# Kernel tuning notes

Measured on AMD Instinct MI355X. Metric: run time of the kernel, lower is better.

The kernel has to match this reference:

```python
import jax, jax.numpy as jnp
import numpy as np

IN_FEATURES = 4096
OUT_FEATURES = 2048
N_GROUPS = 16  # group size = IN_FEATURES // N_GROUPS = 256


def setup_inputs() -> dict:
    key = jax.random.key(0)
    k1, k2, k3, k4 = jax.random.split(key, 4)
    x = jax.random.normal(k1, (8, 64, IN_FEATURES), dtype=jnp.float32)
    # uint8 quantized weights, stored [out, in] as in the torch module
    qweight = jax.random.randint(k2, (OUT_FEATURES, IN_FEATURES), 0, 256).astype(jnp.uint8)
    # per-(out-channel, group) dequant scale and offset; scale ~ (max-min)/255 of rand weights
    qrange = jax.random.uniform(k3, (OUT_FEATURES, N_GROUPS), dtype=jnp.float32) * (2.0 / 255.0)
    qmin = -jax.random.uniform(k4, (OUT_FEATURES, N_GROUPS), dtype=jnp.float32)
    return {"x": x, "qweight": qweight, "qrange": qrange, "qmin": qmin}


def reference(x, qweight, qrange, qmin):
    # out[b,s,o] = sum_i x[b,s,i] * (q[o,i]*qrange[o,g(i)] + qmin[o,g(i)])
    B, S, IN = x.shape
    OUT, G = qrange.shape
    gs = IN // G
    xg = x.reshape(B, S, G, gs)                     # [B,S,G,gs]
    qg = qweight.reshape(OUT, G, gs).astype(x.dtype)  # [O,G,gs]
    # fused per-group dequant matmul: scale folded into the contraction
    out = jnp.einsum('bsgi,ogi,og->bso', xg, qg, qrange)
    # offset term: qmin[o,g] * sum_i_in_group x[b,s,i]
    out = out + jnp.einsum('bsg,og->bso', xg.sum(axis=-1), qmin)
    return out
```

## Files before the change

### kernel.cpp

```cpp
#include <hip/hip_runtime.h>
#include <hip/hip_bf16.h>


#define M_T 512
#define N_T 2048
#define K_T 4096
#define NGRP 16
#define BM 128
#define BN 128
#define BK 64
#define OUT_ELEMS (M_T * N_T)
#define W_ELEMS (N_T * K_T)
#define X_ELEMS (M_T * K_T)

typedef __attribute__((ext_vector_type(8))) short mfrag_t;
typedef __attribute__((ext_vector_type(8))) unsigned short u16x8;
typedef __attribute__((ext_vector_type(4))) float f32x4;

__device__ __forceinline__ unsigned short f2bf(float f) {
  union { __hip_bfloat16 h; unsigned short u; } c;
  c.h = __float2bfloat16(f);
  return c.u;
}

__global__ __launch_bounds__(256) void pack_kernel(
    const float* __restrict__ x, const int* __restrict__ qw,
    const float* __restrict__ qrange, const float* __restrict__ qmin,
    unsigned short* __restrict__ wsW, unsigned short* __restrict__ wsX) {
  const int bid = blockIdx.x;
  const int tid = threadIdx.x;
  if (bid < (W_ELEMS / 8) / 256) {
    const int gidx = bid * 256 + tid;
    const int o = gidx >> 9;
    const int k8 = gidx & 511;
    const int g = k8 >> 5;
    const float sc = qrange[o * NGRP + g];
    const float mn = qmin[o * NGRP + g];
    const int4* q = (const int4*)(qw + ((size_t)o << 12) + (k8 << 3));
    const int4 q0 = q[0], q1 = q[1];
    u16x8 p;
    p[0] = f2bf((float)q0.x * sc + mn); p[1] = f2bf((float)q0.y * sc + mn);
    p[2] = f2bf((float)q0.z * sc + mn); p[3] = f2bf((float)q0.w * sc + mn);
    p[4] = f2bf((float)q1.x * sc + mn); p[5] = f2bf((float)q1.y * sc + mn);
    p[6] = f2bf((float)q1.z * sc + mn); p[7] = f2bf((float)q1.w * sc + mn);
    *(u16x8*)(wsW + ((size_t)gidx << 3)) = p;
  } else {
    const int gidx = (bid - (W_ELEMS / 8) / 256) * 256 + tid;
    const float4* a = (const float4*)(x + ((size_t)gidx << 3));
    const float4 a0 = a[0], a1 = a[1];
    u16x8 p;
    p[0] = f2bf(a0.x); p[1] = f2bf(a0.y); p[2] = f2bf(a0.z); p[3] = f2bf(a0.w);
    p[4] = f2bf(a1.x); p[5] = f2bf(a1.y); p[6] = f2bf(a1.z); p[7] = f2bf(a1.w);
    *(u16x8*)(wsX + ((size_t)gidx << 3)) = p;
  }
}

template <int KSPLIT, bool XCDSWZ>
__global__ __launch_bounds__(512, 4) void dq_gemm_kernel(
    const unsigned short* __restrict__ wsX, const unsigned short* __restrict__ wsW,
    float* __restrict__ dst) {
  constexpr int KC = K_T / KSPLIT;
  constexpr int NTC = KC / BK;

  __shared__ __align__(16) unsigned short As[BM * BK];
  __shared__ __align__(16) unsigned short Bs[BN * BK];

  const int tid = threadIdx.x;
  int xt, yt, kc;
  if (XCDSWZ) {
    const int b = blockIdx.x;
    kc = b & 7;
    const int slot = b >> 3;
    xt = slot & 15;
    yt = slot >> 4;
  } else {
    const int b = blockIdx.x;
    xt = b & 15;
    yt = (b >> 4) & 3;
    kc = b >> 6;
  }
  const int n0 = xt * BN;
  const int m0 = yt * BM;
  const int kbase = kc * KC;

  const int lane = tid & 63;
  const int wv = tid >> 6;
  const int wm = (wv >> 2) * 64;
  const int wn = (wv & 3) * 32;
  const int lr = lane & 15;
  const int lq = lane >> 4;
  const int rxl = lr & 7;

  const int swzcol = (((lane & 7) ^ (lane >> 3)) << 3);
  const int r0 = wv * 16 + (lane >> 3);
  const int r1 = r0 + 8;
  const unsigned short* gA0 = wsX + (size_t)(m0 + r0) * K_T + kbase + swzcol;
  const unsigned short* gA1 = wsX + (size_t)(m0 + r1) * K_T + kbase + swzcol;
  const unsigned short* gB0 = wsW + (size_t)(n0 + r0) * K_T + kbase + swzcol;
  const unsigned short* gB1 = wsW + (size_t)(n0 + r1) * K_T + kbase + swzcol;
  unsigned short* lA0 = &As[wv * 1024];
  unsigned short* lA1 = &As[wv * 1024 + 512];
  unsigned short* lB0 = &Bs[wv * 1024];
  unsigned short* lB1 = &Bs[wv * 1024 + 512];

#define STAGE(T)                                                              \
  do {                                                                        \
    const size_t o_ = (size_t)(T) * BK;                                       \
    __builtin_amdgcn_global_load_lds(                                         \
        (const __attribute__((address_space(1))) void*)(gA0 + o_),            \
        (__attribute__((address_space(3))) void*)lA0, 16, 0, 0);              \
    __builtin_amdgcn_global_load_lds(                                         \
        (const __attribute__((address_space(1))) void*)(gA1 + o_),            \
        (__attribute__((address_space(3))) void*)lA1, 16, 0, 0);              \
    __builtin_amdgcn_global_load_lds(                                         \
        (const __attribute__((address_space(1))) void*)(gB0 + o_),            \
        (__attribute__((address_space(3))) void*)lB0, 16, 0, 0);              \
    __builtin_amdgcn_global_load_lds(                                         \
        (const __attribute__((address_space(1))) void*)(gB1 + o_),            \
        (__attribute__((address_space(3))) void*)lB1, 16, 0, 0);              \
  } while (0)

  f32x4 acc[4][2] = {};

  STAGE(0);
  for (int t = 0; t < NTC; ++t) {
    __syncthreads();

#pragma unroll
    for (int kk = 0; kk < 2; ++kk) {
      const int so = ((kk * 4 + lq) ^ rxl) << 3;
      mfrag_t af[4], bf[2];
#pragma unroll
      for (int fm = 0; fm < 4; ++fm)
        af[fm] = *(const mfrag_t*)&As[(wm + fm * 16 + lr) * BK + so];
#pragma unroll
      for (int fn = 0; fn < 2; ++fn)
        bf[fn] = *(const mfrag_t*)&Bs[(wn + fn * 16 + lr) * BK + so];
#pragma unroll
      for (int fm = 0; fm < 4; ++fm)
#pragma unroll
        for (int fn = 0; fn < 2; ++fn)
          acc[fm][fn] = __builtin_amdgcn_mfma_f32_16x16x32_bf16(af[fm], bf[fn], acc[fm][fn], 0, 0, 0);
    }

    if (t + 1 < NTC) {
      __syncthreads();
      STAGE(t + 1);
    }
  }
#undef STAGE

  float* base = dst + (size_t)kc * OUT_ELEMS;
#pragma unroll
  for (int fm = 0; fm < 4; ++fm) {
#pragma unroll
    for (int fn = 0; fn < 2; ++fn) {
      const int rr = m0 + wm + fm * 16 + lq * 4;
      const int c = n0 + wn + fn * 16 + lr;
      float* op = base + (size_t)rr * N_T + c;
      op[0 * (size_t)N_T] = acc[fm][fn][0];
      op[1 * (size_t)N_T] = acc[fm][fn][1];
      op[2 * (size_t)N_T] = acc[fm][fn][2];
      op[3 * (size_t)N_T] = acc[fm][fn][3];
    }
  }
}

template <int KSPLIT>
__global__ __launch_bounds__(256) void reduce_kernel(const float* __restrict__ ws,
                                                     float* __restrict__ out) {
  const int i4 = blockIdx.x * 256 + threadIdx.x;
  const size_t base = (size_t)i4 * 4;
  float4 a = *(const float4*)(ws + base);
#pragma unroll
  for (int s = 1; s < KSPLIT; ++s) {
    float4 b = *(const float4*)(ws + (size_t)s * OUT_ELEMS + base);
    a.x += b.x; a.y += b.y; a.z += b.z; a.w += b.w;
  }
  *(float4*)(out + base) = a;
}

__global__ void naive_kernel(const float* __restrict__ x, const int* __restrict__ qw,
                             const float* __restrict__ qrange, const float* __restrict__ qmin,
                             float* __restrict__ out) {
  const int idx = blockIdx.x * 256 + threadIdx.x;
  if (idx >= OUT_ELEMS) return;
  const int m = idx / N_T, n = idx % N_T;
  float s = 0.f;
  for (int g = 0; g < NGRP; ++g) {
    const float sc = qrange[n * NGRP + g], mn = qmin[n * NGRP + g];
    float d = 0.f, xs = 0.f;
    for (int k = g * 256; k < (g + 1) * 256; ++k) {
      d += x[(size_t)m * K_T + k] * (float)qw[(size_t)n * K_T + k];
      xs += x[(size_t)m * K_T + k];
    }
    s += d * sc + xs * mn;
  }
  out[idx] = s;
}

extern "C" void kernel_launch(void* const* d_in, const int* in_sizes, int n_in,
                              void* d_out, int out_size, void* d_ws, size_t ws_size,
                              hipStream_t stream) {
  const float* x = (const float*)d_in[0];
  const int* qw = (const int*)d_in[1];
  const float* qr = (const float*)d_in[2];
  const float* qm = (const float*)d_in[3];
  float* out = (float*)d_out;

  constexpr int KS = 8;
  unsigned short* wsW = (unsigned short*)d_ws;
  unsigned short* wsX = wsW + W_ELEMS;
  float* partials = (float*)(wsX + X_ELEMS);
  const size_t need = (size_t)W_ELEMS * 2 + (size_t)X_ELEMS * 2 +
                      (size_t)KS * OUT_ELEMS * sizeof(float);
  if (ws_size >= need) {
    const int packblk = (W_ELEMS / 8) / 256 + (X_ELEMS / 8) / 256;
    pack_kernel<<<packblk, 256, 0, stream>>>(x, qw, qr, qm, wsW, wsX);
    const int nblk = (N_T / BN) * (M_T / BM) * KS;
    dq_gemm_kernel<KS, true><<<nblk, dim3(512, 1, 1), 0, stream>>>(wsX, wsW, partials);
    reduce_kernel<KS><<<OUT_ELEMS / 4 / 256, 256, 0, stream>>>(partials, out);
  } else {
    naive_kernel<<<(OUT_ELEMS + 255) / 256, 256, 0, stream>>>(x, qw, qr, qm, out);
  }
}
```

Before: 35.44 us.

## Use 4 waves per GEMM block with 64x64 warp tiles and inline staging

Cuts the GEMM block from 8 waves to 4. Each wave now computes a 64x64 sub-tile (4x4 MFMA fragments) instead of 64x32, which raises the MFMAs issued per LDS fragment load. Each wave now issues 8 global-to-LDS loads per K-step instead of 4. The prefetch of the next stage, which previously ran between compute steps, is now issued at the top of each iteration and followed immediately by a barrier, so loads no longer overlap compute within a block. The trade is more accumulator registers and fewer waves per block, in exchange for better register reuse and less LDS read traffic.

```diff
diff --git a/kernel.cpp b/kernel.cpp
--- a/kernel.cpp
+++ b/kernel.cpp
@@ -56,7 +56,7 @@
 }
 
 template <int KSPLIT, bool XCDSWZ>
-__global__ __launch_bounds__(512, 4) void dq_gemm_kernel(
+__global__ __launch_bounds__(256, 4) void dq_gemm_kernel(
     const unsigned short* __restrict__ wsX, const unsigned short* __restrict__ wsW,
     float* __restrict__ dst) {
   constexpr int KC = K_T / KSPLIT;
@@ -85,68 +85,56 @@
 
   const int lane = tid & 63;
   const int wv = tid >> 6;
-  const int wm = (wv >> 2) * 64;
-  const int wn = (wv & 3) * 32;
+
+  const int srow8 = lane >> 3;
+  const int scol = (((lane & 7) ^ srow8) << 3);
+  const unsigned short* gA = wsX + (size_t)(m0 + wv * 32 + srow8) * K_T + kbase + scol;
+  const unsigned short* gB = wsW + (size_t)(n0 + wv * 32 + srow8) * K_T + kbase + scol;
+  unsigned short* lA = &As[wv * 32 * BK];
+  unsigned short* lB = &Bs[wv * 32 * BK];
+
+#define STAGE(T)                                                              \
+  do {                                                                        \
+    const size_t o_ = (size_t)(T) * BK;                                       \
+    _Pragma("unroll")                                                         \
+    for (int c_ = 0; c_ < 4; ++c_) {                                          \
+      __builtin_amdgcn_global_load_lds(                                       \
+          (const __attribute__((address_space(1))) void*)(gA + o_ + (size_t)c_ * 8 * K_T), \
+          (__attribute__((address_space(3))) void*)(lA + c_ * 8 * BK), 16, 0, 0); \
+      __builtin_amdgcn_global_load_lds(                                       \
+          (const __attribute__((address_space(1))) void*)(gB + o_ + (size_t)c_ * 8 * K_T), \
+          (__attribute__((address_space(3))) void*)(lB + c_ * 8 * BK), 16, 0, 0); \
+    }                                                                         \
+  } while (0)
+
+  const int wm = (wv >> 1) * 64;
+  const int wn = (wv & 1) * 64;
   const int lr = lane & 15;
   const int lq = lane >> 4;
   const int rxl = lr & 7;
 
-  const int swzcol = (((lane & 7) ^ (lane >> 3)) << 3);
-  const int r0 = wv * 16 + (lane >> 3);
-  const int r1 = r0 + 8;
-  const unsigned short* gA0 = wsX + (size_t)(m0 + r0) * K_T + kbase + swzcol;
-  const unsigned short* gA1 = wsX + (size_t)(m0 + r1) * K_T + kbase + swzcol;
-  const unsigned short* gB0 = wsW + (size_t)(n0 + r0) * K_T + kbase + swzcol;
-  const unsigned short* gB1 = wsW + (size_t)(n0 + r1) * K_T + kbase + swzcol;
-  unsigned short* lA0 = &As[wv * 1024];
-  unsigned short* lA1 = &As[wv * 1024 + 512];
-  unsigned short* lB0 = &Bs[wv * 1024];
-  unsigned short* lB1 = &Bs[wv * 1024 + 512];
-
-#define STAGE(T)                                                              \
-  do {                                                                        \
-    const size_t o_ = (size_t)(T) * BK;                                       \
-    __builtin_amdgcn_global_load_lds(                                         \
-        (const __attribute__((address_space(1))) void*)(gA0 + o_),            \
-        (__attribute__((address_space(3))) void*)lA0, 16, 0, 0);              \
-    __builtin_amdgcn_global_load_lds(                                         \
-        (const __attribute__((address_space(1))) void*)(gA1 + o_),            \
-        (__attribute__((address_space(3))) void*)lA1, 16, 0, 0);              \
-    __builtin_amdgcn_global_load_lds(                                         \
-        (const __attribute__((address_space(1))) void*)(gB0 + o_),            \
-        (__attribute__((address_space(3))) void*)lB0, 16, 0, 0);              \
-    __builtin_amdgcn_global_load_lds(                                         \
-        (const __attribute__((address_space(1))) void*)(gB1 + o_),            \
-        (__attribute__((address_space(3))) void*)lB1, 16, 0, 0);              \
-  } while (0)
-
-  f32x4 acc[4][2] = {};
-
-  STAGE(0);
+  f32x4 acc[4][4] = {};
+
   for (int t = 0; t < NTC; ++t) {
+    if (t > 0) __syncthreads();
+    STAGE(t);
     __syncthreads();
 
 #pragma unroll
     for (int kk = 0; kk < 2; ++kk) {
       const int so = ((kk * 4 + lq) ^ rxl) << 3;
-      mfrag_t af[4], bf[2];
-#pragma unroll
-      for (int fm = 0; fm < 4; ++fm)
-        af[fm] = *(const mfrag_t*)&As[(wm + fm * 16 + lr) * BK + so];
-#pragma unroll
-      for (int fn = 0; fn < 2; ++fn)
+      mfrag_t bf[4];
+#pragma unroll
+      for (int fn = 0; fn < 4; ++fn)
         bf[fn] = *(const mfrag_t*)&Bs[(wn + fn * 16 + lr) * BK + so];
 #pragma unroll
-      for (int fm = 0; fm < 4; ++fm)
-#pragma unroll
-        for (int fn = 0; fn < 2; ++fn)
-          acc[fm][fn] = __builtin_amdgcn_mfma_f32_16x16x32_bf16(af[fm], bf[fn], acc[fm][fn], 0, 0, 0);
+      for (int fm = 0; fm < 4; ++fm) {
+        mfrag_t af = *(const mfrag_t*)&As[(wm + fm * 16 + lr) * BK + so];
+#pragma unroll
+        for (int fn = 0; fn < 4; ++fn)
+          acc[fm][fn] = __builtin_amdgcn_mfma_f32_16x16x32_bf16(af, bf[fn], acc[fm][fn], 0, 0, 0);
+      }
     }
-
-    if (t + 1 < NTC) {
-      __syncthreads();
-      STAGE(t + 1);
-    }
   }
 #undef STAGE
 
@@ -154,7 +142,7 @@
 #pragma unroll
   for (int fm = 0; fm < 4; ++fm) {
 #pragma unroll
-    for (int fn = 0; fn < 2; ++fn) {
+    for (int fn = 0; fn < 4; ++fn) {
       const int rr = m0 + wm + fm * 16 + lq * 4;
       const int c = n0 + wn + fn * 16 + lr;
       float* op = base + (size_t)rr * N_T + c;
@@ -218,7 +206,7 @@
     const int packblk = (W_ELEMS / 8) / 256 + (X_ELEMS / 8) / 256;
     pack_kernel<<<packblk, 256, 0, stream>>>(x, qw, qr, qm, wsW, wsX);
     const int nblk = (N_T / BN) * (M_T / BM) * KS;
-    dq_gemm_kernel<KS, true><<<nblk, dim3(512, 1, 1), 0, stream>>>(wsX, wsW, partials);
+    dq_gemm_kernel<KS, true><<<nblk, dim3(256, 1, 1), 0, stream>>>(wsX, wsW, partials);
     reduce_kernel<KS><<<OUT_ELEMS / 4 / 256, 256, 0, stream>>>(partials, out);
   } else {
     naive_kernel<<<(OUT_ELEMS + 255) / 256, 256, 0, stream>>>(x, qw, qr, qm, out);
```

After: 36.48 us. +2.9%, slower.

## Replace split-K partial buffers and reduce kernel with atomic accumulation

Applied to the files above, without the earlier changes.

The GEMM no longer writes eight full fp32 partial outputs and runs a separate reduce pass. Instead it zeroes the output with a memset and has each split-K block atomically add its tile into the output. This removes the 8x partial-buffer write/read traffic and one kernel launch. The block-to-tile mapping is also remapped so all K-splits of a tile land on the same XCD, keeping the atomics local to one L2. In exchange, atomic float adds make the result order nondeterministic and add atomic contention.

```diff
diff --git a/kernel.cpp b/kernel.cpp
--- a/kernel.cpp
+++ b/kernel.cpp
@@ -55,10 +55,10 @@
   }
 }
 
-template <int KSPLIT, bool XCDSWZ>
+template <int KSPLIT>
 __global__ __launch_bounds__(512, 4) void dq_gemm_kernel(
     const unsigned short* __restrict__ wsX, const unsigned short* __restrict__ wsW,
-    float* __restrict__ dst) {
+    float* __restrict__ out) {
   constexpr int KC = K_T / KSPLIT;
   constexpr int NTC = KC / BK;
 
@@ -66,21 +66,14 @@
   __shared__ __align__(16) unsigned short Bs[BN * BK];
 
   const int tid = threadIdx.x;
-  int xt, yt, kc;
-  if (XCDSWZ) {
-    const int b = blockIdx.x;
-    kc = b & 7;
-    const int slot = b >> 3;
-    xt = slot & 15;
-    yt = slot >> 4;
-  } else {
-    const int b = blockIdx.x;
-    xt = b & 15;
-    yt = (b >> 4) & 3;
-    kc = b >> 6;
-  }
-  const int n0 = xt * BN;
-  const int m0 = yt * BM;
+  const int b = blockIdx.x;
+  const int xcd = b & 7;
+  const int kc = (b >> 3) & 7;
+  const int tile = b >> 6;
+  const int mt = tile & 3;
+  const int nt = 2 * xcd + (tile >> 2);
+  const int n0 = nt * BN;
+  const int m0 = mt * BM;
   const int kbase = kc * KC;
 
   const int lane = tid & 63;
@@ -150,34 +143,19 @@
   }
 #undef STAGE
 
-  float* base = dst + (size_t)kc * OUT_ELEMS;
 #pragma unroll
   for (int fm = 0; fm < 4; ++fm) {
 #pragma unroll
     for (int fn = 0; fn < 2; ++fn) {
       const int rr = m0 + wm + fm * 16 + lq * 4;
       const int c = n0 + wn + fn * 16 + lr;
-      float* op = base + (size_t)rr * N_T + c;
-      op[0 * (size_t)N_T] = acc[fm][fn][0];
-      op[1 * (size_t)N_T] = acc[fm][fn][1];
-      op[2 * (size_t)N_T] = acc[fm][fn][2];
-      op[3 * (size_t)N_T] = acc[fm][fn][3];
-    }
-  }
-}
-
-template <int KSPLIT>
-__global__ __launch_bounds__(256) void reduce_kernel(const float* __restrict__ ws,
-                                                     float* __restrict__ out) {
-  const int i4 = blockIdx.x * 256 + threadIdx.x;
-  const size_t base = (size_t)i4 * 4;
-  float4 a = *(const float4*)(ws + base);
-#pragma unroll
-  for (int s = 1; s < KSPLIT; ++s) {
-    float4 b = *(const float4*)(ws + (size_t)s * OUT_ELEMS + base);
-    a.x += b.x; a.y += b.y; a.z += b.z; a.w += b.w;
-  }
-  *(float4*)(out + base) = a;
+      float* op = out + (size_t)rr * N_T + c;
+      atomicAdd(op + 0 * (size_t)N_T, acc[fm][fn][0]);
+      atomicAdd(op + 1 * (size_t)N_T, acc[fm][fn][1]);
+      atomicAdd(op + 2 * (size_t)N_T, acc[fm][fn][2]);
+      atomicAdd(op + 3 * (size_t)N_T, acc[fm][fn][3]);
+    }
+  }
 }
 
 __global__ void naive_kernel(const float* __restrict__ x, const int* __restrict__ qw,
@@ -211,15 +189,13 @@
   constexpr int KS = 8;
   unsigned short* wsW = (unsigned short*)d_ws;
   unsigned short* wsX = wsW + W_ELEMS;
-  float* partials = (float*)(wsX + X_ELEMS);
-  const size_t need = (size_t)W_ELEMS * 2 + (size_t)X_ELEMS * 2 +
-                      (size_t)KS * OUT_ELEMS * sizeof(float);
+  const size_t need = (size_t)W_ELEMS * 2 + (size_t)X_ELEMS * 2;
   if (ws_size >= need) {
     const int packblk = (W_ELEMS / 8) / 256 + (X_ELEMS / 8) / 256;
     pack_kernel<<<packblk, 256, 0, stream>>>(x, qw, qr, qm, wsW, wsX);
+    hipMemsetAsync(out, 0, (size_t)OUT_ELEMS * sizeof(float), stream);
     const int nblk = (N_T / BN) * (M_T / BM) * KS;
-    dq_gemm_kernel<KS, true><<<nblk, dim3(512, 1, 1), 0, stream>>>(wsX, wsW, partials);
-    reduce_kernel<KS><<<OUT_ELEMS / 4 / 256, 256, 0, stream>>>(partials, out);
+    dq_gemm_kernel<KS><<<nblk, dim3(512, 1, 1), 0, stream>>>(wsX, wsW, out);
   } else {
     naive_kernel<<<(OUT_ELEMS + 255) / 256, 256, 0, stream>>>(x, qw, qr, qm, out);
   }
```

Result: slower. 51.61 us (+45.6%).
